# Optimization experiments

Hardware: AMD Instinct MI355X
Metric: run time of the kernel (lower is better)

The kernel has to match this reference:

```python
import jax, jax.numpy as jnp
import numpy as np

N, E = 50000, 600000
IN, H, OUT = 128, 256, 64
BN_EPS = 1e-5
NEG_SLOPE = 0.01  # F.leaky_relu default


def _gin_conv(x, eps, W1, b1, W2, b2, src, dst):
    # sum aggregation over incoming edges, then 2-layer MLP
    agg = jax.ops.segment_sum(x[src], dst, num_segments=N)  # [N, d]
    h = (1.0 + eps) * x + agg
    h = jax.nn.relu(h @ W1 + b1) @ W2 + b2
    return h


def setup_inputs() -> dict:
    key = jax.random.key(0)
    ks = jax.random.split(key, 16)

    def w(k, shape):
        return (jax.random.normal(k, shape, jnp.float32) / np.sqrt(shape[0])).astype(jnp.float32)

    x = jax.random.normal(ks[0], (N, IN), jnp.float32)
    src = jax.random.randint(ks[1], (E,), 0, N, dtype=jnp.int64)
    dst = jax.random.randint(ks[2], (E,), 0, N, dtype=jnp.int64)
    edge_index = jnp.stack([src, dst])

    return {
        "x": x,
        "edge_index": edge_index,
        # conv0: Linear(IN,H), ReLU, Linear(H,H); trainable eps
        "eps0": jnp.float32(0.0),
        "W01": w(ks[3], (IN, H)), "b01": jnp.zeros((H,), jnp.float32),
        "W02": w(ks[4], (H, H)), "b02": jnp.zeros((H,), jnp.float32),
        # conv1 (middle): eps fixed at 0 (train_eps=False)
        "W11": w(ks[5], (H, H)), "b11": jnp.zeros((H,), jnp.float32),
        "W12": w(ks[6], (H, H)), "b12": jnp.zeros((H,), jnp.float32),
        # conv2 (last): Linear(H,H), ReLU, Linear(H,OUT); trainable eps
        "eps2": jnp.float32(0.0),
        "W21": w(ks[7], (H, H)), "b21": jnp.zeros((H,), jnp.float32),
        "W22": w(ks[8], (H, OUT)), "b22": jnp.zeros((OUT,), jnp.float32),
        # shared BatchNorm1d(H) buffers/params (eval mode)
        "bn_gamma": jnp.ones((H,), jnp.float32),
        "bn_beta": jnp.zeros((H,), jnp.float32),
        "bn_mean": jnp.zeros((H,), jnp.float32),
        "bn_var": jnp.ones((H,), jnp.float32),
    }


def reference(x, edge_index, eps0, W01, b01, W02, b02,
              W11, b11, W12, b12, eps2, W21, b21, W22, b22,
              bn_gamma, bn_beta, bn_mean, bn_var):
    src, dst = edge_index[0], edge_index[1]

    def bn_lrelu(h):
        h = (h - bn_mean) * jax.lax.rsqrt(bn_var + BN_EPS) * bn_gamma + bn_beta
        return jnp.where(h >= 0, h, NEG_SLOPE * h)  # dropout is identity in eval

    h = _gin_conv(x, eps0, W01, b01, W02, b02, src, dst)
    h = bn_lrelu(h)
    h = _gin_conv(h, jnp.float32(0.0), W11, b11, W12, b12, src, dst)
    h = bn_lrelu(h)
    h = _gin_conv(h, eps2, W21, b21, W22, b22, src, dst)
    return h  # [N, OUT]
```

## Files before the change

kernel.cpp:

```cpp
#include <hip/hip_runtime.h>

typedef unsigned short u16;
typedef unsigned int u32;
typedef __attribute__((ext_vector_type(8))) unsigned short u16x8;

constexpr int IN_F = 128;
constexpr int HID  = 256;
constexpr int OUT_F = 64;

static inline int cdiv_i(long long a, long long b) { return (int)((a + b - 1) / b); }

__device__ inline float b2f(u16 h) { return __uint_as_float(((u32)h) << 16); }
__device__ inline u16 f2b(float f) {
    u32 u = __float_as_uint(f);
    u32 r = (u + 0x7FFFu + ((u >> 16) & 1u)) >> 16;
    return (u16)r;
}
__device__ inline float4 ld4(const float* p) { return *reinterpret_cast<const float4*>(p); }

__global__ __launch_bounds__(256) void deg_count_kernel(
    const int* __restrict__ ei, int* __restrict__ deg, int E)
{
    int e = blockIdx.x * blockDim.x + threadIdx.x;
    if (e >= E) return;
    atomicAdd(&deg[ei[E + e]], 1);
}

__global__ __launch_bounds__(1024) void block_scan_kernel(
    const int* __restrict__ deg, int* __restrict__ row_ptr,
    int* __restrict__ blksum, int Nn)
{
    __shared__ int buf[1024];
    int i = blockIdx.x * 1024 + threadIdx.x;
    int v = (i < Nn) ? deg[i] : 0;
    buf[threadIdx.x] = v;
    __syncthreads();
    for (int off = 1; off < 1024; off <<= 1) {
        int t = (threadIdx.x >= off) ? buf[threadIdx.x - off] : 0;
        __syncthreads();
        buf[threadIdx.x] += t;
        __syncthreads();
    }
    if (i < Nn) row_ptr[i] = buf[threadIdx.x] - v;
    if (threadIdx.x == 1023) blksum[blockIdx.x] = buf[1023];
}

__global__ __launch_bounds__(1024) void scan_blksums_kernel(
    int* __restrict__ blksum, int nblk)
{
    __shared__ int buf[1024];
    int v = (threadIdx.x < nblk) ? blksum[threadIdx.x] : 0;
    buf[threadIdx.x] = v;
    __syncthreads();
    for (int off = 1; off < 1024; off <<= 1) {
        int t = (threadIdx.x >= off) ? buf[threadIdx.x - off] : 0;
        __syncthreads();
        buf[threadIdx.x] += t;
        __syncthreads();
    }
    if (threadIdx.x < nblk) blksum[threadIdx.x] = buf[threadIdx.x] - v;
}

__global__ __launch_bounds__(1024) void add_offsets_kernel(
    int* __restrict__ row_ptr, int* __restrict__ cursor,
    const int* __restrict__ blksum, int Nn, int E)
{
    int i = blockIdx.x * 1024 + threadIdx.x;
    if (i < Nn) {
        int r = row_ptr[i] + blksum[i >> 10];
        row_ptr[i] = r;
        cursor[i]  = r;
    } else if (i == Nn) {
        row_ptr[Nn] = E;
    }
}

__global__ __launch_bounds__(256) void csr_fill_kernel(
    const int* __restrict__ ei, int* __restrict__ cursor,
    int* __restrict__ csr_src, int E)
{
    int e = blockIdx.x * blockDim.x + threadIdx.x;
    if (e >= E) return;
    int d = ei[E + e];
    int pos = atomicAdd(&cursor[d], 1);
    csr_src[pos] = ei[e];
}

__global__ __launch_bounds__(256) void xconv_kernel(
    const float4* __restrict__ in, ushort4* __restrict__ out, long long total4)
{
    long long i = (long long)blockIdx.x * blockDim.x + threadIdx.x;
    if (i >= total4) return;
    float4 v = in[i];
    ushort4 o;
    o.x = f2b(v.x); o.y = f2b(v.y); o.z = f2b(v.z); o.w = f2b(v.w);
    out[i] = o;
}

__global__ __launch_bounds__(256) void wconv_all_kernel(
    const float* __restrict__ W01, const float* __restrict__ W02,
    const float* __restrict__ W11, const float* __restrict__ W12,
    const float* __restrict__ W21, const float* __restrict__ W22,
    u16* __restrict__ Wt01, u16* __restrict__ Wt02,
    u16* __restrict__ Wt11, u16* __restrict__ Wt12,
    u16* __restrict__ Wt21, u16* __restrict__ Wt22)
{
    int id = blockIdx.x * blockDim.x + threadIdx.x;
    const float* W; u16* Wt; int kshift, NC;
    if (id < 32768)                  { W = W01; Wt = Wt01; kshift = 7; NC = 256; }
    else if ((id -= 32768) < 65536)  { W = W02; Wt = Wt02; kshift = 8; NC = 256; }
    else if ((id -= 65536) < 65536)  { W = W11; Wt = Wt11; kshift = 8; NC = 256; }
    else if ((id -= 65536) < 65536)  { W = W12; Wt = Wt12; kshift = 8; NC = 256; }
    else if ((id -= 65536) < 65536)  { W = W21; Wt = Wt21; kshift = 8; NC = 256; }
    else if ((id -= 65536) < 16384)  { W = W22; Wt = Wt22; kshift = 8; NC = 64;  }
    else return;
    int K = 1 << kshift;
    int n = id >> kshift;
    int k = id & (K - 1);
    Wt[id] = f2b(W[(long long)k * NC + n]);
}

__global__ __launch_bounds__(256) void agg256_bf16(
    const u16x8* __restrict__ x, const int* __restrict__ row_ptr,
    const int* __restrict__ csr_src, const float* __restrict__ eps_ptr,
    u16x8* __restrict__ out, int Nn)
{
    int n = blockIdx.x * 4 + (threadIdx.x >> 6);
    if (n >= Nn) return;
    int lane = threadIdx.x & 63;
    int grp = lane >> 5;
    int sl  = lane & 31;
    size_t off = (size_t)n * 32 + sl;
    float acc[8];
    if (grp == 0) {
        float e1 = 1.0f + (eps_ptr ? *eps_ptr : 0.0f);
        u16x8 xv = x[off];
#pragma unroll
        for (int i = 0; i < 8; ++i) acc[i] = e1 * b2f(xv[i]);
    } else {
#pragma unroll
        for (int i = 0; i < 8; ++i) acc[i] = 0.0f;
    }
    int end = row_ptr[n + 1];
    int j = row_ptr[n] + grp;
    for (; j + 2 < end; j += 4) {
        int s0 = csr_src[j], s1 = csr_src[j + 2];
        u16x8 v0 = x[(size_t)s0 * 32 + sl];
        u16x8 v1 = x[(size_t)s1 * 32 + sl];
#pragma unroll
        for (int i = 0; i < 8; ++i) acc[i] += b2f(v0[i]) + b2f(v1[i]);
    }
    if (j < end) {
        u16x8 v = x[(size_t)csr_src[j] * 32 + sl];
#pragma unroll
        for (int i = 0; i < 8; ++i) acc[i] += b2f(v[i]);
    }
#pragma unroll
    for (int i = 0; i < 8; ++i) acc[i] += __shfl_xor(acc[i], 32, 64);
    if (grp == 0) {
        u16x8 o;
#pragma unroll
        for (int i = 0; i < 8; ++i) o[i] = f2b(acc[i]);
        out[off] = o;
    }
}

__global__ __launch_bounds__(256) void agg128_bf16(
    const u16x8* __restrict__ x, const int* __restrict__ row_ptr,
    const int* __restrict__ csr_src, const float* __restrict__ eps_ptr,
    u16x8* __restrict__ out, int Nn)
{
    int n = blockIdx.x * 4 + (threadIdx.x >> 6);
    if (n >= Nn) return;
    int lane = threadIdx.x & 63;
    int grp = lane >> 4;
    int sl  = lane & 15;
    size_t off = (size_t)n * 16 + sl;
    float acc[8];
    if (grp == 0) {
        float e1 = 1.0f + (eps_ptr ? *eps_ptr : 0.0f);
        u16x8 xv = x[off];
#pragma unroll
        for (int i = 0; i < 8; ++i) acc[i] = e1 * b2f(xv[i]);
    } else {
#pragma unroll
        for (int i = 0; i < 8; ++i) acc[i] = 0.0f;
    }
    int end = row_ptr[n + 1];
    int j = row_ptr[n] + grp;
    for (; j + 4 < end; j += 8) {
        int s0 = csr_src[j], s1 = csr_src[j + 4];
        u16x8 v0 = x[(size_t)s0 * 16 + sl];
        u16x8 v1 = x[(size_t)s1 * 16 + sl];
#pragma unroll
        for (int i = 0; i < 8; ++i) acc[i] += b2f(v0[i]) + b2f(v1[i]);
    }
    if (j < end) {
        u16x8 v = x[(size_t)csr_src[j] * 16 + sl];
#pragma unroll
        for (int i = 0; i < 8; ++i) acc[i] += b2f(v[i]);
    }
#pragma unroll
    for (int i = 0; i < 8; ++i) {
        acc[i] += __shfl_xor(acc[i], 16, 64);
        acc[i] += __shfl_xor(acc[i], 32, 64);
    }
    if (grp == 0) {
        u16x8 o;
#pragma unroll
        for (int i = 0; i < 8; ++i) o[i] = f2b(acc[i]);
        out[off] = o;
    }
}

using bf16x8 = __attribute__((ext_vector_type(8))) short;
using f32x4  = __attribute__((ext_vector_type(4))) float;

__device__ inline void gload_lds16(const void* g, void* l) {
    __builtin_amdgcn_global_load_lds(
        (const __attribute__((address_space(1))) u32*)g,
        (__attribute__((address_space(3))) u32*)l, 16, 0, 0);
}

template <int KIN, int NOUT, int FUSE2, bool OF32>
__global__ __launch_bounds__(512, 4) void mlp_fused(
    const u16* __restrict__ A, const u16* __restrict__ W1t,
    const float* __restrict__ b1,
    const u16* __restrict__ W2t, const float* __restrict__ b2,
    const float* __restrict__ bn_g, const float* __restrict__ bn_b,
    const float* __restrict__ bn_m, const float* __restrict__ bn_v,
    void* __restrict__ Cout, int M)
{
    constexpr int GPR = KIN / 8;
    __shared__ u16 As[64 * KIN];
    __shared__ u16 Hl[64 * 256];

    const int tid  = threadIdx.x;
    const int wv   = tid >> 6;
    const int lane = tid & 63;
    const int l15  = lane & 15, l4 = lane >> 4;
    const int m0   = blockIdx.x * 64;

#pragma unroll
    for (int it = 0; it < KIN / 64; ++it) {
        int inst = it * 8 + wv;
        int gi = inst * 64 + lane;
        int row = gi / GPR;
        int g = gi & (GPR - 1);
        int gs = g ^ (row & 7);
        int grow = m0 + row; if (grow >= M) grow = M - 1;
        gload_lds16(A + (size_t)grow * KIN + gs * 8, As + inst * 512);
    }
    __syncthreads();

    f32x4 acc1[4][2] = {};
#pragma unroll
    for (int kt = 0; kt < KIN / 64; ++kt) {
#pragma unroll
        for (int kk = 0; kk < 2; ++kk) {
            int g = kt * 8 + kk * 4 + l4;
            bf16x8 af[4], wf[2];
#pragma unroll
            for (int n = 0; n < 2; ++n) {
                int wrow = wv * 32 + n * 16 + l15;
                wf[n] = *(const bf16x8*)(W1t + (size_t)wrow * KIN + g * 8);
            }
#pragma unroll
            for (int m = 0; m < 4; ++m) {
                int row = m * 16 + l15;
                af[m] = *(const bf16x8*)(As + row * KIN + ((g ^ (row & 7)) * 8));
            }
#pragma unroll
            for (int m = 0; m < 4; ++m)
#pragma unroll
                for (int n = 0; n < 2; ++n)
                    acc1[m][n] = __builtin_amdgcn_mfma_f32_16x16x32_bf16(
                        wf[n], af[m], acc1[m][n], 0, 0, 0);
        }
    }
#pragma unroll
    for (int m = 0; m < 4; ++m) {
        int arow = m * 16 + l15;
#pragma unroll
        for (int n = 0; n < 2; ++n) {
            int hcol = wv * 32 + n * 16 + l4 * 4;
            float4 bv = ld4(b1 + hcol);
            float v0 = fmaxf(acc1[m][n][0] + bv.x, 0.f);
            float v1 = fmaxf(acc1[m][n][1] + bv.y, 0.f);
            float v2 = fmaxf(acc1[m][n][2] + bv.z, 0.f);
            float v3 = fmaxf(acc1[m][n][3] + bv.w, 0.f);
            u32 p0 = (u32)f2b(v0) | ((u32)f2b(v1) << 16);
            u32 p1 = (u32)f2b(v2) | ((u32)f2b(v3) << 16);
            int g = hcol >> 3;
            u16* dst = Hl + arow * 256 + ((g ^ (arow & 7)) * 8) + (hcol & 7);
            *reinterpret_cast<uint2*>(dst) = make_uint2(p0, p1);
        }
    }
    __syncthreads();

    constexpr int MF2 = (NOUT == 256) ? 4 : 2;
    constexpr int NF2 = (NOUT == 256) ? 2 : 1;
    const int rbase = (NOUT == 256) ? 0 : (wv >> 2) * 32;
    const int cbase = (NOUT == 256) ? wv * 32 : (wv & 3) * 16;

    f32x4 acc2[MF2][NF2] = {};
#pragma unroll
    for (int kt = 0; kt < 4; ++kt) {
#pragma unroll
        for (int kk = 0; kk < 2; ++kk) {
            int g = kt * 8 + kk * 4 + l4;
            bf16x8 hf[MF2], wf[NF2];
#pragma unroll
            for (int n = 0; n < NF2; ++n) {
                int wrow = cbase + n * 16 + l15;
                wf[n] = *(const bf16x8*)(W2t + (size_t)wrow * 256 + g * 8);
            }
#pragma unroll
            for (int m = 0; m < MF2; ++m) {
                int row = rbase + m * 16 + l15;
                hf[m] = *(const bf16x8*)(Hl + row * 256 + ((g ^ (row & 7)) * 8));
            }
#pragma unroll
            for (int m = 0; m < MF2; ++m)
#pragma unroll
                for (int n = 0; n < NF2; ++n)
                    acc2[m][n] = __builtin_amdgcn_mfma_f32_16x16x32_bf16(
                        wf[n], hf[m], acc2[m][n], 0, 0, 0);
        }
    }

#pragma unroll
    for (int m = 0; m < MF2; ++m) {
        int grow = m0 + rbase + m * 16 + l15;
        if (grow >= M) continue;
#pragma unroll
        for (int n = 0; n < NF2; ++n) {
            int col = cbase + n * 16 + l4 * 4;
            float4 bv = ld4(b2 + col);
            float v0 = acc2[m][n][0] + bv.x;
            float v1 = acc2[m][n][1] + bv.y;
            float v2 = acc2[m][n][2] + bv.z;
            float v3 = acc2[m][n][3] + bv.w;
            if (FUSE2 == 1) {
                float4 g = ld4(bn_g + col), be = ld4(bn_b + col);
                float4 mm = ld4(bn_m + col), vv = ld4(bn_v + col);
                float s0 = g.x * rsqrtf(vv.x + 1e-5f);
                float s1 = g.y * rsqrtf(vv.y + 1e-5f);
                float s2 = g.z * rsqrtf(vv.z + 1e-5f);
                float s3 = g.w * rsqrtf(vv.w + 1e-5f);
                v0 = fmaf(v0, s0, be.x - mm.x * s0);
                v1 = fmaf(v1, s1, be.y - mm.y * s1);
                v2 = fmaf(v2, s2, be.z - mm.z * s2);
                v3 = fmaf(v3, s3, be.w - mm.w * s3);
                v0 = v0 >= 0.f ? v0 : 0.01f * v0;
                v1 = v1 >= 0.f ? v1 : 0.01f * v1;
                v2 = v2 >= 0.f ? v2 : 0.01f * v2;
                v3 = v3 >= 0.f ? v3 : 0.01f * v3;
            }
            if (OF32) {
                float4 o = make_float4(v0, v1, v2, v3);
                *reinterpret_cast<float4*>((float*)Cout + (size_t)grow * NOUT + col) = o;
            } else {
                u32 p0 = (u32)f2b(v0) | ((u32)f2b(v1) << 16);
                u32 p1 = (u32)f2b(v2) | ((u32)f2b(v3) << 16);
                *reinterpret_cast<uint2*>((u16*)Cout + (size_t)grow * NOUT + col) =
                    make_uint2(p0, p1);
            }
        }
    }
}

extern "C" void kernel_launch(void* const* d_in, const int* in_sizes, int n_in,
                              void* d_out, int out_size, void* d_ws, size_t ws_size,
                              hipStream_t stream)
{
    const float* x    = (const float*)d_in[0];
    const int*   ei   = (const int*)d_in[1];
    const float* eps0 = (const float*)d_in[2];
    const float* W01  = (const float*)d_in[3];
    const float* b01  = (const float*)d_in[4];
    const float* W02  = (const float*)d_in[5];
    const float* b02  = (const float*)d_in[6];
    const float* W11  = (const float*)d_in[7];
    const float* b11  = (const float*)d_in[8];
    const float* W12  = (const float*)d_in[9];
    const float* b12  = (const float*)d_in[10];
    const float* eps2 = (const float*)d_in[11];
    const float* W21  = (const float*)d_in[12];
    const float* b21  = (const float*)d_in[13];
    const float* W22  = (const float*)d_in[14];
    const float* b22  = (const float*)d_in[15];
    const float* bn_g = (const float*)d_in[16];
    const float* bn_b = (const float*)d_in[17];
    const float* bn_m = (const float*)d_in[18];
    const float* bn_v = (const float*)d_in[19];

    const int Nn = in_sizes[0] / IN_F;
    const int E  = in_sizes[1] / 2;

    u16* P = (u16*)d_ws;
    u16* Q = P + (size_t)Nn * HID;
    u16* Xb = Q + (size_t)Nn * HID;
    u16* Wt01 = Xb + (size_t)Nn * IN_F;
    u16* Wt02 = Wt01 + HID * IN_F;
    u16* Wt11 = Wt02 + HID * HID;
    u16* Wt12 = Wt11 + HID * HID;
    u16* Wt21 = Wt12 + HID * HID;
    u16* Wt22 = Wt21 + HID * HID;
    int* row_ptr = (int*)(Wt22 + OUT_F * HID);
    int* cursor  = row_ptr + (Nn + 1);
    int* deg     = cursor + Nn;
    int* blksum  = deg + Nn;
    int* csr_src = blksum + 1024;

    dim3 blk(256);
    const int nwave_blocks = cdiv_i(Nn, 4);
    const int nscan = cdiv_i(Nn, 1024);

    hipMemsetAsync(deg, 0, (size_t)Nn * sizeof(int), stream);
    deg_count_kernel<<<cdiv_i(E, 256), blk, 0, stream>>>(ei, deg, E);
    block_scan_kernel<<<nscan, 1024, 0, stream>>>(deg, row_ptr, blksum, Nn);
    scan_blksums_kernel<<<1, 1024, 0, stream>>>(blksum, nscan);
    add_offsets_kernel<<<cdiv_i(Nn + 1, 1024), 1024, 0, stream>>>(
        row_ptr, cursor, blksum, Nn, E);
    csr_fill_kernel<<<cdiv_i(E, 256), blk, 0, stream>>>(ei, cursor, csr_src, E);

    xconv_kernel<<<cdiv_i((long long)Nn * IN_F / 4, 256), blk, 0, stream>>>(
        (const float4*)x, (ushort4*)Xb, (long long)Nn * IN_F / 4);
    wconv_all_kernel<<<cdiv_i(32768 + 4 * 65536 + 16384, 256), blk, 0, stream>>>(
        W01, W02, W11, W12, W21, W22, Wt01, Wt02, Wt11, Wt12, Wt21, Wt22);

    const int mlp_blocks = cdiv_i(Nn, 64);
    const dim3 blk512(512);

    agg128_bf16<<<nwave_blocks, blk, 0, stream>>>(
        (const u16x8*)Xb, row_ptr, csr_src, eps0, (u16x8*)P, Nn);
    mlp_fused<128, 256, 1, false><<<mlp_blocks, blk512, 0, stream>>>(
        P, Wt01, b01, Wt02, b02, bn_g, bn_b, bn_m, bn_v, Q, Nn);

    agg256_bf16<<<nwave_blocks, blk, 0, stream>>>(
        (const u16x8*)Q, row_ptr, csr_src, nullptr, (u16x8*)P, Nn);
    mlp_fused<256, 256, 1, false><<<mlp_blocks, blk512, 0, stream>>>(
        P, Wt11, b11, Wt12, b12, bn_g, bn_b, bn_m, bn_v, Q, Nn);

    agg256_bf16<<<nwave_blocks, blk, 0, stream>>>(
        (const u16x8*)Q, row_ptr, csr_src, eps2, (u16x8*)P, Nn);
    mlp_fused<256, 64, 2, true><<<mlp_blocks, blk512, 0, stream>>>(
        P, Wt21, b21, Wt22, b22, nullptr, nullptr, nullptr, nullptr, d_out, Nn);
}
```

Measured before the change: 336.1 us.

## Stage MLP weights through double-buffered LDS, halve row tile, unroll aggregation, merge conversions

The fused MLP kernel now stages W1/W2 tiles into LDS with a double-buffered 32-wide K pipeline instead of having every wave read weights straight from global memory. It also shrinks the row tile from 64 to 32, which doubles the block count. The 256-wide aggregation loop is unrolled to four gathers per iteration for more memory-level parallelism, and the x and weight bf16 conversion kernels are merged into a single launch. The cost is more __syncthreads per block and less reuse of each weight tile across rows.

```diff
diff --git a/kernel.cpp b/kernel.cpp
--- a/kernel.cpp
+++ b/kernel.cpp
@@ -86,18 +86,8 @@
     csr_src[pos] = ei[e];
 }
 
-__global__ __launch_bounds__(256) void xconv_kernel(
-    const float4* __restrict__ in, ushort4* __restrict__ out, long long total4)
-{
-    long long i = (long long)blockIdx.x * blockDim.x + threadIdx.x;
-    if (i >= total4) return;
-    float4 v = in[i];
-    ushort4 o;
-    o.x = f2b(v.x); o.y = f2b(v.y); o.z = f2b(v.z); o.w = f2b(v.w);
-    out[i] = o;
-}
-
-__global__ __launch_bounds__(256) void wconv_all_kernel(
+__global__ __launch_bounds__(256) void conv_all_kernel(
+    const float* __restrict__ x, u16* __restrict__ Xb, int nx4,
     const float* __restrict__ W01, const float* __restrict__ W02,
     const float* __restrict__ W11, const float* __restrict__ W12,
     const float* __restrict__ W21, const float* __restrict__ W22,
@@ -106,6 +96,14 @@
     u16* __restrict__ Wt21, u16* __restrict__ Wt22)
 {
     int id = blockIdx.x * blockDim.x + threadIdx.x;
+    if (id < nx4) {
+        float4 v = reinterpret_cast<const float4*>(x)[id];
+        ushort4 o;
+        o.x = f2b(v.x); o.y = f2b(v.y); o.z = f2b(v.z); o.w = f2b(v.w);
+        reinterpret_cast<ushort4*>(Xb)[id] = o;
+        return;
+    }
+    id -= nx4;
     const float* W; u16* Wt; int kshift, NC;
     if (id < 32768)                  { W = W01; Wt = Wt01; kshift = 7; NC = 256; }
     else if ((id -= 32768) < 65536)  { W = W02; Wt = Wt02; kshift = 8; NC = 256; }
@@ -143,14 +141,18 @@
     }
     int end = row_ptr[n + 1];
     int j = row_ptr[n] + grp;
-    for (; j + 2 < end; j += 4) {
-        int s0 = csr_src[j], s1 = csr_src[j + 2];
+    for (; j + 6 < end; j += 8) {
+        int s0 = csr_src[j],     s1 = csr_src[j + 2];
+        int s2 = csr_src[j + 4], s3 = csr_src[j + 6];
         u16x8 v0 = x[(size_t)s0 * 32 + sl];
         u16x8 v1 = x[(size_t)s1 * 32 + sl];
-#pragma unroll
-        for (int i = 0; i < 8; ++i) acc[i] += b2f(v0[i]) + b2f(v1[i]);
-    }
-    if (j < end) {
+        u16x8 v2 = x[(size_t)s2 * 32 + sl];
+        u16x8 v3 = x[(size_t)s3 * 32 + sl];
+#pragma unroll
+        for (int i = 0; i < 8; ++i)
+            acc[i] += (b2f(v0[i]) + b2f(v1[i])) + (b2f(v2[i]) + b2f(v3[i]));
+    }
+    for (; j < end; j += 2) {
         u16x8 v = x[(size_t)csr_src[j] * 32 + sl];
 #pragma unroll
         for (int i = 0; i < 8; ++i) acc[i] += b2f(v[i]);
@@ -223,7 +225,7 @@
 }
 
 template <int KIN, int NOUT, int FUSE2, bool OF32>
-__global__ __launch_bounds__(512, 4) void mlp_fused(
+__global__ __launch_bounds__(512, 4) void mlp2(
     const u16* __restrict__ A, const u16* __restrict__ W1t,
     const float* __restrict__ b1,
     const u16* __restrict__ W2t, const float* __restrict__ b2,
@@ -232,54 +234,94 @@
     void* __restrict__ Cout, int M)
 {
     constexpr int GPR = KIN / 8;
-    __shared__ u16 As[64 * KIN];
-    __shared__ u16 Hl[64 * 256];
+    constexpr int KT1 = KIN / 32;
+    constexpr int KT2 = 256 / 32;
+    __shared__ __align__(16) u16 Wb[2][256 * 32];
+    __shared__ __align__(16) u16 Al[32 * KIN];
+    __shared__ __align__(16) u16 Hl[32 * 256];
 
     const int tid  = threadIdx.x;
     const int wv   = tid >> 6;
     const int lane = tid & 63;
     const int l15  = lane & 15, l4 = lane >> 4;
-    const int m0   = blockIdx.x * 64;
-
-#pragma unroll
-    for (int it = 0; it < KIN / 64; ++it) {
-        int inst = it * 8 + wv;
-        int gi = inst * 64 + lane;
-        int row = gi / GPR;
-        int g = gi & (GPR - 1);
-        int gs = g ^ (row & 7);
-        int grow = m0 + row; if (grow >= M) grow = M - 1;
-        gload_lds16(A + (size_t)grow * KIN + gs * 8, As + inst * 512);
-    }
+    const int m0   = blockIdx.x * 32;
+
+    {
+        constexpr int AI = (32 * GPR) / 64;
+        constexpr int IPW = (AI + 7) / 8;
+#pragma unroll
+        for (int i = 0; i < IPW; ++i) {
+            int inst = wv * IPW + i;
+            if (inst < AI) {
+                int gi = inst * 64 + lane;
+                int row = gi / GPR;
+                int g = gi % GPR;
+                int grow = m0 + row; if (grow >= M) grow = M - 1;
+                gload_lds16(A + (size_t)grow * KIN + ((g ^ (row & 7)) * 8),
+                            Al + inst * 512);
+            }
+        }
+    }
+    auto stageW1 = [&](int kt, int buf) {
+#pragma unroll
+        for (int i = 0; i < 2; ++i) {
+            int inst = wv * 2 + i;
+            int gi = inst * 64 + lane;
+            int row = gi >> 2;
+            int g = gi & 3;
+            gload_lds16(W1t + (size_t)row * KIN + kt * 32 + ((g ^ (row & 3)) * 8),
+                        Wb[buf] + inst * 512);
+        }
+    };
+    auto stageW2 = [&](int kt, int buf) {
+        constexpr int WI = (NOUT * 4) / 64;
+        constexpr int IPW = (WI + 7) / 8;
+#pragma unroll
+        for (int i = 0; i < IPW; ++i) {
+            int inst = wv * IPW + i;
+            if (inst < WI) {
+                int gi = inst * 64 + lane;
+                int row = gi >> 2;
+                int g = gi & 3;
+                gload_lds16(W2t + (size_t)row * 256 + kt * 32 + ((g ^ (row & 3)) * 8),
+                            Wb[buf] + inst * 512);
+            }
+        }
+    };
+
+    stageW1(0, 0);
     __syncthreads();
-
-    f32x4 acc1[4][2] = {};
-#pragma unroll
-    for (int kt = 0; kt < KIN / 64; ++kt) {
-#pragma unroll
-        for (int kk = 0; kk < 2; ++kk) {
-            int g = kt * 8 + kk * 4 + l4;
-            bf16x8 af[4], wf[2];
-#pragma unroll
-            for (int n = 0; n < 2; ++n) {
-                int wrow = wv * 32 + n * 16 + l15;
-                wf[n] = *(const bf16x8*)(W1t + (size_t)wrow * KIN + g * 8);
-            }
-#pragma unroll
-            for (int m = 0; m < 4; ++m) {
-                int row = m * 16 + l15;
-                af[m] = *(const bf16x8*)(As + row * KIN + ((g ^ (row & 7)) * 8));
-            }
-#pragma unroll
-            for (int m = 0; m < 4; ++m)
-#pragma unroll
-                for (int n = 0; n < 2; ++n)
-                    acc1[m][n] = __builtin_amdgcn_mfma_f32_16x16x32_bf16(
-                        wf[n], af[m], acc1[m][n], 0, 0, 0);
-        }
-    }
-#pragma unroll
-    for (int m = 0; m < 4; ++m) {
+    int buf = 0;
+
+    f32x4 acc1[2][2] = {};
+#pragma unroll
+    for (int kt = 0; kt < KT1; ++kt) {
+        if (kt + 1 < KT1) stageW1(kt + 1, buf ^ 1);
+        else              stageW2(0, buf ^ 1);
+        bf16x8 wf[2], af[2];
+#pragma unroll
+        for (int n = 0; n < 2; ++n) {
+            int wrow = wv * 32 + n * 16 + l15;
+            wf[n] = *(const bf16x8*)(Wb[buf] + wrow * 32 + ((l4 ^ (wrow & 3)) * 8));
+        }
+#pragma unroll
+        for (int m = 0; m < 2; ++m) {
+            int arow = m * 16 + l15;
+            int g = kt * 4 + l4;
+            af[m] = *(const bf16x8*)(Al + arow * GPR * 8 + ((g ^ (arow & 7)) * 8));
+        }
+#pragma unroll
+        for (int m = 0; m < 2; ++m)
+#pragma unroll
+            for (int n = 0; n < 2; ++n)
+                acc1[m][n] = __builtin_amdgcn_mfma_f32_16x16x32_bf16(
+                    wf[n], af[m], acc1[m][n], 0, 0, 0);
+        __syncthreads();
+        buf ^= 1;
+    }
+
+#pragma unroll
+    for (int m = 0; m < 2; ++m) {
         int arow = m * 16 + l15;
 #pragma unroll
         for (int n = 0; n < 2; ++n) {
@@ -298,43 +340,45 @@
     }
     __syncthreads();
 
-    constexpr int MF2 = (NOUT == 256) ? 4 : 2;
-    constexpr int NF2 = (NOUT == 256) ? 2 : 1;
-    const int rbase = (NOUT == 256) ? 0 : (wv >> 2) * 32;
+    constexpr int MF = (NOUT == 256) ? 2 : 1;
+    constexpr int NF = (NOUT == 256) ? 2 : 1;
+    const int rbase = (NOUT == 256) ? 0 : (wv >> 2) * 16;
     const int cbase = (NOUT == 256) ? wv * 32 : (wv & 3) * 16;
 
-    f32x4 acc2[MF2][NF2] = {};
-#pragma unroll
-    for (int kt = 0; kt < 4; ++kt) {
-#pragma unroll
-        for (int kk = 0; kk < 2; ++kk) {
-            int g = kt * 8 + kk * 4 + l4;
-            bf16x8 hf[MF2], wf[NF2];
-#pragma unroll
-            for (int n = 0; n < NF2; ++n) {
-                int wrow = cbase + n * 16 + l15;
-                wf[n] = *(const bf16x8*)(W2t + (size_t)wrow * 256 + g * 8);
-            }
-#pragma unroll
-            for (int m = 0; m < MF2; ++m) {
-                int row = rbase + m * 16 + l15;
-                hf[m] = *(const bf16x8*)(Hl + row * 256 + ((g ^ (row & 7)) * 8));
-            }
-#pragma unroll
-            for (int m = 0; m < MF2; ++m)
-#pragma unroll
-                for (int n = 0; n < NF2; ++n)
-                    acc2[m][n] = __builtin_amdgcn_mfma_f32_16x16x32_bf16(
-                        wf[n], hf[m], acc2[m][n], 0, 0, 0);
-        }
-    }
-
-#pragma unroll
-    for (int m = 0; m < MF2; ++m) {
+    f32x4 acc2[MF][NF] = {};
+#pragma unroll
+    for (int kt = 0; kt < KT2; ++kt) {
+        if (kt + 1 < KT2) stageW2(kt + 1, buf ^ 1);
+        bf16x8 wf[NF], hf[MF];
+#pragma unroll
+        for (int n = 0; n < NF; ++n) {
+            int wrow = cbase + n * 16 + l15;
+            wf[n] = *(const bf16x8*)(Wb[buf] + wrow * 32 + ((l4 ^ (wrow & 3)) * 8));
+        }
+#pragma unroll
+        for (int m = 0; m < MF; ++m) {
+            int arow = rbase + m * 16 + l15;
+            int g = kt * 4 + l4;
+            hf[m] = *(const bf16x8*)(Hl + arow * 256 + ((g ^ (arow & 7)) * 8));
+        }
+#pragma unroll
+        for (int m = 0; m < MF; ++m)
+#pragma unroll
+            for (int n = 0; n < NF; ++n)
+                acc2[m][n] = __builtin_amdgcn_mfma_f32_16x16x32_bf16(
+                    wf[n], hf[m], acc2[m][n], 0, 0, 0);
+        if (kt + 1 < KT2) {
+            __syncthreads();
+            buf ^= 1;
+        }
+    }
+
+#pragma unroll
+    for (int m = 0; m < MF; ++m) {
         int grow = m0 + rbase + m * 16 + l15;
         if (grow >= M) continue;
 #pragma unroll
-        for (int n = 0; n < NF2; ++n) {
+        for (int n = 0; n < NF; ++n) {
             int col = cbase + n * 16 + l4 * 4;
             float4 bv = ld4(b2 + col);
             float v0 = acc2[m][n][0] + bv.x;
@@ -342,12 +386,12 @@
             float v2 = acc2[m][n][2] + bv.z;
             float v3 = acc2[m][n][3] + bv.w;
             if (FUSE2 == 1) {
-                float4 g = ld4(bn_g + col), be = ld4(bn_b + col);
+                float4 g4 = ld4(bn_g + col), be = ld4(bn_b + col);
                 float4 mm = ld4(bn_m + col), vv = ld4(bn_v + col);
-                float s0 = g.x * rsqrtf(vv.x + 1e-5f);
-                float s1 = g.y * rsqrtf(vv.y + 1e-5f);
-                float s2 = g.z * rsqrtf(vv.z + 1e-5f);
-                float s3 = g.w * rsqrtf(vv.w + 1e-5f);
+                float s0 = g4.x * rsqrtf(vv.x + 1e-5f);
+                float s1 = g4.y * rsqrtf(vv.y + 1e-5f);
+                float s2 = g4.z * rsqrtf(vv.z + 1e-5f);
+                float s3 = g4.w * rsqrtf(vv.w + 1e-5f);
                 v0 = fmaf(v0, s0, be.x - mm.x * s0);
                 v1 = fmaf(v1, s1, be.y - mm.y * s1);
                 v2 = fmaf(v2, s2, be.z - mm.z * s2);
@@ -359,12 +403,13 @@
             }
             if (OF32) {
                 float4 o = make_float4(v0, v1, v2, v3);
-                *reinterpret_cast<float4*>((float*)Cout + (size_t)grow * NOUT + col) = o;
+                *reinterpret_cast<float4*>(
+                    (float*)Cout + (size_t)grow * NOUT + col) = o;
             } else {
                 u32 p0 = (u32)f2b(v0) | ((u32)f2b(v1) << 16);
                 u32 p1 = (u32)f2b(v2) | ((u32)f2b(v3) << 16);
-                *reinterpret_cast<uint2*>((u16*)Cout + (size_t)grow * NOUT + col) =
-                    make_uint2(p0, p1);
+                *reinterpret_cast<uint2*>(
+                    (u16*)Cout + (size_t)grow * NOUT + col) = make_uint2(p0, p1);
             }
         }
     }
@@ -425,26 +470,29 @@
         row_ptr, cursor, blksum, Nn, E);
     csr_fill_kernel<<<cdiv_i(E, 256), blk, 0, stream>>>(ei, cursor, csr_src, E);
 
-    xconv_kernel<<<cdiv_i((long long)Nn * IN_F / 4, 256), blk, 0, stream>>>(
-        (const float4*)x, (ushort4*)Xb, (long long)Nn * IN_F / 4);
-    wconv_all_kernel<<<cdiv_i(32768 + 4 * 65536 + 16384, 256), blk, 0, stream>>>(
-        W01, W02, W11, W12, W21, W22, Wt01, Wt02, Wt11, Wt12, Wt21, Wt22);
-
-    const int mlp_blocks = cdiv_i(Nn, 64);
+    {
+        int nx4 = Nn * IN_F / 4;
+        long long tot = (long long)nx4 + (32768 + 4 * 65536 + 16384);
+        conv_all_kernel<<<cdiv_i(tot, 256), blk, 0, stream>>>(
+            x, Xb, nx4, W01, W02, W11, W12, W21, W22,
+            Wt01, Wt02, Wt11, Wt12, Wt21, Wt22);
+    }
+
+    const int mlp_blocks = cdiv_i(Nn, 32);
     const dim3 blk512(512);
 
     agg128_bf16<<<nwave_blocks, blk, 0, stream>>>(
         (const u16x8*)Xb, row_ptr, csr_src, eps0, (u16x8*)P, Nn);
-    mlp_fused<128, 256, 1, false><<<mlp_blocks, blk512, 0, stream>>>(
+    mlp2<128, 256, 1, false><<<mlp_blocks, blk512, 0, stream>>>(
         P, Wt01, b01, Wt02, b02, bn_g, bn_b, bn_m, bn_v, Q, Nn);
 
     agg256_bf16<<<nwave_blocks, blk, 0, stream>>>(
         (const u16x8*)Q, row_ptr, csr_src, nullptr, (u16x8*)P, Nn);
-    mlp_fused<256, 256, 1, false><<<mlp_blocks, blk512, 0, stream>>>(
+    mlp2<256, 256, 1, false><<<mlp_blocks, blk512, 0, stream>>>(
         P, Wt11, b11, Wt12, b12, bn_g, bn_b, bn_m, bn_v, Q, Nn);
 
     agg256_bf16<<<nwave_blocks, blk, 0, stream>>>(
         (const u16x8*)Q, row_ptr, csr_src, eps2, (u16x8*)P, Nn);
-    mlp_fused<256, 64, 2, true><<<mlp_blocks, blk512, 0, stream>>>(
+    mlp2<256, 64, 2, true><<<mlp_blocks, blk512, 0, stream>>>(
         P, Wt21, b21, Wt22, b22, nullptr, nullptr, nullptr, nullptr, d_out, Nn);
 }
```

Result: faster. 324.2 us (-3.6%).
